# Performance work log

Measured on AMD Instinct MI355X. Metric: run time of the kernel, lower is better.

The kernel has to match this reference:

```python
import jax, jax.numpy as jnp
import numpy as np

DIM = 1024
H = 8            # heads (light and heavy)
DH = 64          # dim_head
W = 64           # local attention window (light_window_size // 2)
NQ = 512         # num_heavy_tokens_q
NKV = 1024       # num_heavy_tokens_kv
EPS = 1.0        # coor descent eps
NITERS = 50      # coor descent iters
FETCH = 9.0 / 8.0
SCALE = DH ** -0.5


def _ln(x, w, b):
    m = x.mean(-1, keepdims=True)
    v = ((x - m) ** 2).mean(-1, keepdims=True)
    return (x - m) * jax.lax.rsqrt(v + 1e-5) * w + b


def _rms(x, g):
    n = jnp.maximum(jnp.linalg.norm(x, axis=-1, keepdims=True), 1e-12)
    return x / n * np.sqrt(DIM).astype(np.float32) * g


def local_attn(x, Wqkv, Wout):
    # LocalMHA, non-causal, look_backward=1, look_forward=1, window W
    b, n, _ = x.shape
    nw = n // W
    qkv = x @ Wqkv.T                      # [b,n,3*H*DH]
    q, k, v = jnp.split(qkv, 3, axis=-1)
    def towin(t):
        return t.reshape(b, nw, W, H, DH).transpose(0, 3, 1, 2, 4)  # [b,h,nw,w,dh]
    q, k, v = map(towin, (q, k, v))
    def expand(t):  # gather prev/cur/next windows -> [b,h,nw,3w,dh]
        tp = jnp.pad(t, ((0, 0), (0, 0), (1, 1), (0, 0), (0, 0)))
        return jnp.concatenate([tp[:, :, :-2], tp[:, :, 1:-1], tp[:, :, 2:]], axis=3)
    ke, ve = expand(k), expand(v)
    sim = jnp.einsum('bhnid,bhnjd->bhnij', q, ke) * SCALE
    win = jnp.arange(nw)
    valid = jnp.concatenate([
        jnp.repeat((win > 0)[:, None], W, 1),
        jnp.ones((nw, W), bool),
        jnp.repeat((win < nw - 1)[:, None], W, 1)], axis=1)  # [nw,3w]
    sim = jnp.where(valid[None, None, :, None, :], sim, -1e9)
    attn = jax.nn.softmax(sim, axis=-1)
    o = jnp.einsum('bhnij,bhnjd->bhnid', attn, ve)
    o = o.transpose(0, 2, 3, 1, 4).reshape(b, n, H * DH)
    return o @ Wout.T


def route(x, routing_token, num_tokens):
    # CoordinateDescentRouter with num_routing_tokens=1, straight_through=True
    s = jnp.einsum('bnd,rd->brn', x, routing_token).reshape(x.shape[0], x.shape[1])
    n = s.shape[-1]
    logk = jnp.log(jnp.asarray(min(num_tokens * FETCH, float(n)), s.dtype))
    def body(ab, _):
        a, bb = ab
        a = EPS * (logk - jax.nn.logsumexp((s + bb) / EPS, axis=-1, keepdims=True))
        bb = -jax.nn.relu(s + a)
        return (a, bb), None
    (a, bb), _ = jax.lax.scan(body, (jnp.zeros((s.shape[0], 1), s.dtype), -s), None, length=NITERS)
    scores = jnp.exp((s + a + bb) / EPS)
    sel_scores, sel_idx = jax.lax.top_k(scores, num_tokens)
    # straight-through: forward value 1.0, gradient of identity
    sel_scores = sel_scores + jax.lax.stop_gradient(1.0 - sel_scores)
    return sel_scores, sel_idx


def heavy_attn(xq, ctx, scores_kv, gamma, Wq, Wkv, Wout, null_kv):
    b = xq.shape[0]
    xq = _rms(xq, gamma)
    ctx = _rms(ctx, gamma)
    q = (xq @ Wq.T).reshape(b, -1, H, DH).transpose(0, 2, 1, 3)           # [b,h,nq,dh]
    kv = (ctx @ Wkv.T).reshape(b, -1, H, 2 * DH).transpose(0, 2, 1, 3)    # [b,h,nkv,2dh]
    k, v = kv[..., :DH], kv[..., DH:]
    v = v * scores_kv[:, None, :, None]
    nk = jnp.broadcast_to(null_kv[0][None, :, None, :], (b, H, 1, DH))
    nv = jnp.broadcast_to(null_kv[1][None, :, None, :], (b, H, 1, DH))
    k = jnp.concatenate([nk, k], axis=2)
    v = jnp.concatenate([nv, v], axis=2)
    sim = jnp.einsum('bhid,bhjd->bhij', q, k) * SCALE
    attn = jax.nn.softmax(sim, axis=-1)
    o = jnp.einsum('bhij,bhjd->bhid', attn, v)
    o = o.transpose(0, 2, 1, 3).reshape(b, -1, H * DH)
    return o @ Wout.T


def setup_inputs() -> dict:
    key = jax.random.key(0)
    ks = jax.random.split(key, 12)
    D, IN = DIM, H * DH
    w = lambda k, shape: jax.random.normal(k, shape, jnp.float32) * 0.02
    return {
        'x': jax.random.normal(ks[0], (4, 4096, D), jnp.float32),
        'ln_w': jnp.ones((D,), jnp.float32),
        'ln_b': jnp.zeros((D,), jnp.float32),
        'Wqkv': w(ks[1], (3 * IN, D)),
        'Wout_l': w(ks[2], (D, IN)),
        'rt_q': jax.random.normal(ks[3], (1, D), jnp.float32),
        'rt_kv': jax.random.normal(ks[4], (1, D), jnp.float32),
        'gamma': jnp.ones((D,), jnp.float32),
        'Wq': w(ks[5], (IN, D)),
        'Wkv': w(ks[6], (2 * IN, D)),
        'Wout_h': w(ks[7], (D, IN)),
        'null_kv': jax.random.normal(ks[8], (2, H, DH), jnp.float32),
        'null_q': jax.random.normal(ks[9], (D,), jnp.float32),
    }


def reference(x, ln_w, ln_b, Wqkv, Wout_l, rt_q, rt_kv, gamma, Wq, Wkv, Wout_h, null_kv, null_q):
    b, n, d = x.shape
    light = local_attn(_ln(x, ln_w, ln_b), Wqkv, Wout_l)
    sq, iq = route(x, rt_q, NQ)
    skv, ikv = route(x, rt_kv, NKV)
    br = jnp.arange(b)[:, None]
    xq = x[br, iq]          # gather routed queries  [b,NQ,d]
    xkv = x[br, ikv]        # gather routed kv       [b,NKV,d]
    heavy = heavy_attn(xq, xkv, skv, gamma, Wq, Wkv, Wout_h, null_kv)
    heavy = heavy * sq[..., None]
    out = jnp.broadcast_to(null_q[None, None, :], (b, n, d))
    out = out.at[br, iq].set(heavy)   # scatter heavy branch back
    return out + light
```

## Files before the change

kernel.cpp:

```cpp
#include <hip/hip_runtime.h>
#include <hip/hip_bf16.h>

typedef __attribute__((ext_vector_type(8))) short bv8;
typedef __attribute__((ext_vector_type(4))) float fv4;
typedef __hip_bfloat16 bf16;

#define MFMA16(a,b,c) __builtin_amdgcn_mfma_f32_16x16x32_bf16((a),(b),(c),0,0,0)
#define GLOAD_LDS(gp, lp) __builtin_amdgcn_global_load_lds( \
    (const __attribute__((address_space(1))) void*)(gp), \
    (__attribute__((address_space(3))) void*)(lp), 16, 0, 0)

template<int NW>
__device__ __forceinline__ float blockReduceSumF(float v) {
  #pragma unroll
  for (int m = 1; m < 64; m <<= 1) v += __shfl_xor(v, m, 64);
  __shared__ float sm[NW];
  if ((threadIdx.x & 63) == 0) sm[threadIdx.x >> 6] = v;
  __syncthreads();
  float t = 0.f;
  #pragma unroll
  for (int i = 0; i < NW; ++i) t += sm[i];
  __syncthreads();
  return t;
}

template<int NW>
__device__ __forceinline__ double blockReduceMaxD(double v) {
  #pragma unroll
  for (int m = 1; m < 64; m <<= 1) v = fmax(v, __shfl_xor(v, m, 64));
  __shared__ double sm[NW];
  if ((threadIdx.x & 63) == 0) sm[threadIdx.x >> 6] = v;
  __syncthreads();
  double t = sm[0];
  #pragma unroll
  for (int i = 1; i < NW; ++i) t = fmax(t, sm[i]);
  __syncthreads();
  return t;
}

__global__ __launch_bounds__(256)
void prep_kernel(const float* __restrict__ x, const float* __restrict__ lnw,
                 const float* __restrict__ lnb, const float* __restrict__ rtq,
                 const float* __restrict__ rtkv, bf16* __restrict__ lnout,
                 double* __restrict__ s,
                 const float* __restrict__ a0, const float* __restrict__ a1,
                 const float* __restrict__ a2, const float* __restrict__ a3,
                 const float* __restrict__ a4,
                 bf16* __restrict__ b0, bf16* __restrict__ b1, bf16* __restrict__ b2,
                 bf16* __restrict__ b3, bf16* __restrict__ b4,
                 int* __restrict__ posq) {
  const int bid = blockIdx.x;
  if (bid < 16384) {
    const int r = bid;
    const float* xr = x + (size_t)r * 1024;
    float v4[4]; float ssum = 0.f;
    double dq = 0.0, dk = 0.0;
    #pragma unroll
    for (int i = 0; i < 4; ++i) {
      int d = threadIdx.x + i * 256;
      float v = xr[d];
      v4[i] = v; ssum += v;
      dq += (double)v * (double)rtq[d];
      dk += (double)v * (double)rtkv[d];
    }
    ssum = blockReduceSumF<4>(ssum);
    const float mean = ssum * (1.0f / 1024.0f);
    float vs = 0.f;
    #pragma unroll
    for (int i = 0; i < 4; ++i) { float d = v4[i] - mean; vs += d * d; }
    vs = blockReduceSumF<4>(vs);
    const float rstd = 1.0f / sqrtf(vs * (1.0f / 1024.0f) + 1e-5f);
    #pragma unroll
    for (int m = 1; m < 64; m <<= 1) { dq += __shfl_xor(dq, m, 64); dk += __shfl_xor(dk, m, 64); }
    __shared__ double smq[4], smk[4];
    if ((threadIdx.x & 63) == 0) { smq[threadIdx.x >> 6] = dq; smk[threadIdx.x >> 6] = dk; }
    __syncthreads();
    if (threadIdx.x == 0) {
      s[r] = smq[0] + smq[1] + smq[2] + smq[3];
      s[16384 + r] = smk[0] + smk[1] + smk[2] + smk[3];
    }
    bf16* orow = lnout + (size_t)r * 1024;
    #pragma unroll
    for (int i = 0; i < 4; ++i) {
      int d = threadIdx.x + i * 256;
      orow[d] = __float2bfloat16((v4[i] - mean) * rstd * lnw[d] + lnb[d]);
    }
  } else if (bid < 18432) {
    size_t g = ((size_t)(bid - 16384) * 256 + threadIdx.x) * 8;
    const float* src; bf16* dst; size_t off;
    if (g < 1572864)      { src = a0; dst = b0; off = g; }
    else if (g < 2097152) { src = a1; dst = b1; off = g - 1572864; }
    else if (g < 2621440) { src = a2; dst = b2; off = g - 2097152; }
    else if (g < 3670016) { src = a3; dst = b3; off = g - 2621440; }
    else                  { src = a4; dst = b4; off = g - 3670016; }
    float4 v0 = *(const float4*)(src + off);
    float4 v1 = *(const float4*)(src + off + 4);
    bv8 o;
    ((bf16*)&o)[0] = __float2bfloat16(v0.x); ((bf16*)&o)[1] = __float2bfloat16(v0.y);
    ((bf16*)&o)[2] = __float2bfloat16(v0.z); ((bf16*)&o)[3] = __float2bfloat16(v0.w);
    ((bf16*)&o)[4] = __float2bfloat16(v1.x); ((bf16*)&o)[5] = __float2bfloat16(v1.y);
    ((bf16*)&o)[6] = __float2bfloat16(v1.z); ((bf16*)&o)[7] = __float2bfloat16(v1.w);
    *(bv8*)(dst + off) = o;
  } else {
    int i0 = (bid - 18432) * 1024 + threadIdx.x * 4;
    posq[i0] = -1; posq[i0 + 1] = -1; posq[i0 + 2] = -1; posq[i0 + 3] = -1;
  }
}

template<int EPI>
__device__ __forceinline__ void gemm_core(
    const bf16* __restrict__ A, const bf16* __restrict__ B, void* __restrict__ Cout,
    int N, int K, int row0, int col0, bf16* As, bf16* Bs,
    const int* __restrict__ posq, const float* __restrict__ nullq) {
  const int tid = threadIdx.x;
  const int lane = tid & 63, w = tid >> 6;
  const int wr = w >> 1, wc = w & 1;
  const int lrow = lane & 15, lk = (lane >> 4) * 8;
  fv4 acc[4][4];
  #pragma unroll
  for (int m = 0; m < 4; ++m)
    #pragma unroll
    for (int n = 0; n < 4; ++n) acc[m][n] = (fv4){0.f, 0.f, 0.f, 0.f};
  const int ob0 = w * 2048;
  for (int k0 = 0; k0 < K; k0 += 32) {
    #pragma unroll
    for (int t = 0; t < 2; ++t) {
      int ob = ob0 + t * 1024;
      int ofl = ob + lane * 16;
      int r = ofl >> 6, c8 = ((ofl >> 4) & 3) * 8;
      GLOAD_LDS(A + (size_t)(row0 + r) * K + k0 + c8, (char*)As + ob);
      GLOAD_LDS(B + (size_t)(col0 + r) * K + k0 + c8, (char*)Bs + ob);
    }
    __syncthreads();
    bv8 af[4], bfr[4];
    #pragma unroll
    for (int m = 0; m < 4; ++m) af[m] = *(bv8*)&As[(wr * 64 + m * 16 + lrow) * 32 + lk];
    #pragma unroll
    for (int n = 0; n < 4; ++n) bfr[n] = *(bv8*)&Bs[(wc * 64 + n * 16 + lrow) * 32 + lk];
    #pragma unroll
    for (int m = 0; m < 4; ++m)
      #pragma unroll
      for (int n = 0; n < 4; ++n)
        acc[m][n] = MFMA16(af[m], bfr[n], acc[m][n]);
    __syncthreads();
  }
  #pragma unroll
  for (int m = 0; m < 4; ++m) {
    int gr0 = row0 + wr * 64 + m * 16 + (lane >> 4) * 4;
    #pragma unroll
    for (int n = 0; n < 4; ++n) {
      int gc = col0 + wc * 64 + n * 16 + lrow;
      #pragma unroll
      for (int r = 0; r < 4; ++r) {
        int grow = gr0 + r;
        float vv = acc[m][n][r];
        if (EPI == 0) {
          ((bf16*)Cout)[(size_t)grow * N + gc] = __float2bfloat16(vv);
        } else {
          float add = (posq[grow] >= 0) ? 0.0f : nullq[gc];
          ((float*)Cout)[(size_t)grow * N + gc] = vv + add;
        }
      }
    }
  }
}

__device__ __forceinline__ void xcd_remap(int d, int gx, int& row0, int& col0) {
  int q = d >> 3;
  col0 = (q % gx) * 128;
  row0 = ((d & 7) + 8 * (q / gx)) * 128;
}

__global__ __launch_bounds__(256)
void qkv_route_kernel(const bf16* __restrict__ ln, const bf16* __restrict__ Wqkv,
                      bf16* __restrict__ qkv,
                      const double* __restrict__ s_all, int* __restrict__ iq,
                      int* __restrict__ ikv, int* __restrict__ posq,
                      unsigned long long* __restrict__ keys_ws) {
  __shared__ alignas(16) bf16 As[128 * 32];
  __shared__ alignas(16) bf16 Bs[128 * 32];
  __shared__ int scn[256];
  __shared__ double red[4];
  const int bid = blockIdx.x;
  const int tid = threadIdx.x;
  if (bid >= 8) {
    int row0, col0;
    xcd_remap(bid - 8, 12, row0, col0);
    gemm_core<0>(ln, Wqkv, qkv, 1536, 1024, row0, col0, As, Bs, nullptr, nullptr);
  } else {
    const int route = bid >> 2, b = bid & 3;
    const double* s = s_all + route * 16384 + b * 4096;
    const double Kk = (route == 0) ? 576.0 : 1152.0;
    const int KSEL = (route == 0) ? 512 : 1024;
    const int lane = tid & 63, wid = tid >> 6;
    double sv[16];
    #pragma unroll
    for (int i = 0; i < 16; ++i) sv[i] = s[tid * 16 + i];
    double mx = sv[0];
    #pragma unroll
    for (int i = 1; i < 16; ++i) mx = fmax(mx, sv[i]);
    mx = blockReduceMaxD<4>(mx);
    double ev[16];
    #pragma unroll
    for (int i = 0; i < 16; ++i) ev[i] = exp(sv[i] - mx);
    double z = (4096.0 / Kk) * exp(-mx);
    for (int it = 1; it < 50; ++it) {
      double t0 = 0.0, t1 = 0.0;
      #pragma unroll
      for (int i = 0; i < 16; i += 2) { t0 += fmin(ev[i], z); t1 += fmin(ev[i + 1], z); }
      double t = t0 + t1;
      #pragma unroll
      for (int m = 1; m < 64; m <<= 1) t += __shfl_xor(t, m, 64);
      if (lane == 0) red[wid] = t;
      __syncthreads();
      z = (red[0] + red[1] + red[2] + red[3]) / Kk;
      __syncthreads();
    }
    const double a = -mx - log(z);
    float scf[16]; int m16 = 0;
    #pragma unroll
    for (int i = 0; i < 16; ++i) {
      scf[i] = (float)exp(fmin(sv[i] + a, 0.0));
      m16 += (scf[i] == 1.0f) ? 1 : 0;
    }
    scn[tid] = m16;
    __syncthreads();
    for (int off = 1; off < 256; off <<= 1) {
      int v = (tid >= off) ? scn[tid - off] : 0;
      __syncthreads();
      scn[tid] += v;
      __syncthreads();
    }
    const int total = scn[255];
    const int excl = scn[tid] - m16;
    if (total >= KSEL) {
      int rk = excl;
      #pragma unroll
      for (int i = 0; i < 16; ++i) {
        if (scf[i] == 1.0f) {
          if (rk < KSEL) {
            int idx = tid * 16 + i;
            if (route == 0) { iq[b * 512 + rk] = idx; posq[b * 4096 + idx] = rk; }
            else            { ikv[b * 1024 + rk] = idx; }
          }
          rk++;
        }
      }
    } else {
      unsigned long long* keys = keys_ws + (size_t)bid * 4096;
      #pragma unroll
      for (int i = 0; i < 16; ++i) {
        unsigned bits = __float_as_uint(scf[i]);
        keys[tid * 16 + i] = ((unsigned long long)(~bits) << 32) | (unsigned long long)(tid * 16 + i);
      }
      for (int k = 2; k <= 4096; k <<= 1) {
        for (int j = k >> 1; j > 0; j >>= 1) {
          __syncthreads();
          for (int t = tid; t < 2048; t += 256) {
            int i2 = ((t & ~(j - 1)) << 1) | (t & (j - 1));
            int ip = i2 + j;
            unsigned long long av = keys[i2], bvv = keys[ip];
            bool up = ((i2 & k) == 0);
            if (up ? (av > bvv) : (av < bvv)) { keys[i2] = bvv; keys[ip] = av; }
          }
        }
      }
      __syncthreads();
      for (int j2 = tid; j2 < KSEL; j2 += 256) {
        int idx = (int)(keys[j2] & 0xFFFFFFFFull);
        if (route == 0) { iq[b * 512 + j2] = idx; posq[b * 4096 + idx] = j2; }
        else            { ikv[b * 1024 + j2] = idx; }
      }
    }
  }
}

__global__ __launch_bounds__(256)
void la_gather_kernel(const bf16* __restrict__ qkv, bf16* __restrict__ olight,
                      const float* __restrict__ x, const float* __restrict__ gamma,
                      const int* __restrict__ iq, const int* __restrict__ ikv,
                      bf16* __restrict__ xq, bf16* __restrict__ xkv) {
  __shared__ bf16 Qs[64][72], Ks[64][72], Vts[64][72], Ps[64][72];
  const int tid = threadIdx.x;
  if (blockIdx.x < 2048) {
    const int w = blockIdx.x & 63, h = (blockIdx.x >> 6) & 7, b = blockIdx.x >> 9;
    const int lane = tid & 63, wv = tid >> 6;
    const int lrow = lane & 15, lkg = lane >> 4;
    {
      const size_t baseq = ((size_t)(b * 4096 + w * 64)) * 1536 + h * 64;
      #pragma unroll
      for (int v = 0; v < 2; ++v) {
        int vec = tid + v * 256; int i = vec >> 3, dd = (vec & 7) * 8;
        *(bv8*)&Qs[i][dd] = *(const bv8*)&qkv[baseq + (size_t)i * 1536 + dd];
      }
    }
    fv4 oacc[4];
    float m_run[4], l_run[4];
    #pragma unroll
    for (int n = 0; n < 4; ++n) oacc[n] = (fv4){0.f, 0.f, 0.f, 0.f};
    #pragma unroll
    for (int r = 0; r < 4; ++r) { m_run[r] = -INFINITY; l_run[r] = 0.f; }
    for (int c = 0; c < 3; ++c) {
      int sw = w - 1 + c;
      if (sw < 0 || sw >= 64) continue;
      __syncthreads();
      const size_t bkv = ((size_t)(b * 4096 + sw * 64)) * 1536 + h * 64;
      #pragma unroll
      for (int v = 0; v < 2; ++v) {
        int vec = tid + v * 256; int i = vec >> 3, dd = (vec & 7) * 8;
        *(bv8*)&Ks[i][dd] = *(const bv8*)&qkv[bkv + 512 + (size_t)i * 1536 + dd];
      }
      #pragma unroll
      for (int v = 0; v < 2; ++v) {
        int vec = tid + v * 256; int j = vec >> 3, d0 = (vec & 7) * 8;
        bv8 val = *(const bv8*)&qkv[bkv + 1024 + (size_t)j * 1536 + d0];
        #pragma unroll
        for (int i = 0; i < 8; ++i) Vts[d0 + i][j] = ((bf16*)&val)[i];
      }
      __syncthreads();
      fv4 sa[4];
      #pragma unroll
      for (int n = 0; n < 4; ++n) {
        sa[n] = (fv4){0.f, 0.f, 0.f, 0.f};
        #pragma unroll
        for (int ks = 0; ks < 2; ++ks) {
          bv8 aq = *(bv8*)&Qs[wv * 16 + lrow][lkg * 8 + ks * 32];
          bv8 bk = *(bv8*)&Ks[n * 16 + lrow][lkg * 8 + ks * 32];
          sa[n] = MFMA16(aq, bk, sa[n]);
        }
      }
      float mc[4];
      #pragma unroll
      for (int r = 0; r < 4; ++r) {
        #pragma unroll
        for (int n = 0; n < 4; ++n) sa[n][r] *= 0.125f;
        mc[r] = fmaxf(fmaxf(sa[0][r], sa[1][r]), fmaxf(sa[2][r], sa[3][r]));
      }
      #pragma unroll
      for (int m = 1; m < 16; m <<= 1)
        #pragma unroll
        for (int r = 0; r < 4; ++r) mc[r] = fmaxf(mc[r], __shfl_xor(mc[r], m, 64));
      float p[4][4], ls[4];
      #pragma unroll
      for (int r = 0; r < 4; ++r) {
        float mn = fmaxf(m_run[r], mc[r]);
        float scl = expf(m_run[r] - mn);
        ls[r] = 0.f;
        #pragma unroll
        for (int n = 0; n < 4; ++n) { p[n][r] = expf(sa[n][r] - mn); ls[r] += p[n][r]; }
        m_run[r] = mn;
        l_run[r] *= scl;
        #pragma unroll
        for (int n = 0; n < 4; ++n) oacc[n][r] *= scl;
      }
      #pragma unroll
      for (int m = 1; m < 16; m <<= 1)
        #pragma unroll
        for (int r = 0; r < 4; ++r) ls[r] += __shfl_xor(ls[r], m, 64);
      #pragma unroll
      for (int r = 0; r < 4; ++r) l_run[r] += ls[r];
      #pragma unroll
      for (int n = 0; n < 4; ++n)
        #pragma unroll
        for (int r = 0; r < 4; ++r)
          Ps[wv * 16 + lkg * 4 + r][n * 16 + lrow] = __float2bfloat16(p[n][r]);
      __syncthreads();
      #pragma unroll
      for (int n = 0; n < 4; ++n)
        #pragma unroll
        for (int ks = 0; ks < 2; ++ks) {
          bv8 ap = *(bv8*)&Ps[wv * 16 + lrow][lkg * 8 + ks * 32];
          bv8 bvv = *(bv8*)&Vts[n * 16 + lrow][lkg * 8 + ks * 32];
          oacc[n] = MFMA16(ap, bvv, oacc[n]);
        }
    }
    const size_t ob = ((size_t)(b * 4096 + w * 64 + wv * 16)) * 512 + h * 64;
    #pragma unroll
    for (int n = 0; n < 4; ++n)
      #pragma unroll
      for (int r = 0; r < 4; ++r) {
        int row = lkg * 4 + r;
        olight[ob + (size_t)row * 512 + n * 16 + lrow] = __float2bfloat16(oacc[n][r] / l_run[r]);
      }
  } else {
    const int gid = blockIdx.x - 2048;
    const float* src; bf16* dst;
    if (gid < 2048) {
      int b = gid >> 9, j = gid & 511;
      int tok = iq[b * 512 + j];
      src = x + ((size_t)(b * 4096 + tok)) * 1024;
      dst = xq + (size_t)gid * 1024;
    } else {
      int id = gid - 2048;
      int b = id >> 10, j = id & 1023;
      int tok = ikv[b * 1024 + j];
      src = x + ((size_t)(b * 4096 + tok)) * 1024;
      dst = xkv + (size_t)id * 1024;
    }
    float v4[4]; float ss = 0.f;
    #pragma unroll
    for (int i = 0; i < 4; ++i) { v4[i] = src[tid + i * 256]; ss += v4[i] * v4[i]; }
    ss = blockReduceSumF<4>(ss);
    const float nrm = fmaxf(sqrtf(ss), 1e-12f);
    const float scl = 32.0f / nrm;
    #pragma unroll
    for (int i = 0; i < 4; ++i) {
      int d = tid + i * 256;
      dst[d] = __float2bfloat16(v4[i] * scl * gamma[d]);
    }
  }
}

__global__ __launch_bounds__(256)
void lightout_wqkv_kernel(const bf16* __restrict__ ol, const bf16* __restrict__ Woutl,
                          float* __restrict__ out,
                          const int* __restrict__ posq, const float* __restrict__ nq,
                          const bf16* __restrict__ xkv, const bf16* __restrict__ Wkv,
                          bf16* __restrict__ kvh,
                          const bf16* __restrict__ xq, const bf16* __restrict__ Wq,
                          bf16* __restrict__ qh) {
  __shared__ alignas(16) bf16 As[128 * 32];
  __shared__ alignas(16) bf16 Bs[128 * 32];
  const int bid = blockIdx.x;
  int row0, col0;
  if (bid < 256) {
    xcd_remap(bid, 8, row0, col0);
    gemm_core<0>(xkv, Wkv, kvh, 1024, 1024, row0, col0, As, Bs, nullptr, nullptr);
  } else if (bid < 320) {
    xcd_remap(bid - 256, 4, row0, col0);
    gemm_core<0>(xq, Wq, qh, 512, 1024, row0, col0, As, Bs, nullptr, nullptr);
  } else {
    xcd_remap(bid - 320, 8, row0, col0);
    gemm_core<2>(ol, Woutl, out, 1024, 512, row0, col0, As, Bs, posq, nq);
  }
}

__global__ __launch_bounds__(256)
void heavy_attn_split_kernel(const bf16* __restrict__ qh, const bf16* __restrict__ kvh,
                             const float* __restrict__ nkv, bf16* __restrict__ o_part,
                             float* __restrict__ ml_part) {
  const int qt = blockIdx.x, h = blockIdx.y;
  const int b = blockIdx.z >> 2, s = blockIdx.z & 3;
  const int tid = threadIdx.x;
  const int lane = tid & 63, wv = tid >> 6;
  const int lrow = lane & 15, lkg = lane >> 4;
  __shared__ bf16 Qs[64][72], Ks[64][72], Vts[64][72], Ps[64][72];
  {
    const size_t baseq = ((size_t)(b * 512 + qt * 64)) * 512 + h * 64;
    #pragma unroll
    for (int v = 0; v < 2; ++v) {
      int vec = tid + v * 256; int i = vec >> 3, dd = (vec & 7) * 8;
      *(bv8*)&Qs[i][dd] = *(const bv8*)&qh[baseq + (size_t)i * 512 + dd];
    }
  }
  fv4 oacc[4];
  float m_run[4], l_run[4];
  #pragma unroll
  for (int n = 0; n < 4; ++n) oacc[n] = (fv4){0.f, 0.f, 0.f, 0.f};
  #pragma unroll
  for (int r = 0; r < 4; ++r) { m_run[r] = -INFINITY; l_run[r] = 0.f; }
  const int cs = (s == 0) ? 0 : (s * 4 + 1);
  const int ce = s * 4 + 5;
  for (int c = cs; c < ce; ++c) {
    __syncthreads();
    #pragma unroll
    for (int v = 0; v < 2; ++v) {
      int vec = tid + v * 256; int j = vec >> 3, dd = (vec & 7) * 8;
      int kvg = c * 64 + j;
      bv8 val;
      if (kvg >= 1 && kvg <= 1024) {
        val = *(const bv8*)&kvh[((size_t)(b * 1024 + kvg - 1)) * 1024 + h * 128 + dd];
      } else if (kvg == 0) {
        #pragma unroll
        for (int t = 0; t < 8; ++t) ((bf16*)&val)[t] = __float2bfloat16(nkv[h * 64 + dd + t]);
      } else {
        #pragma unroll
        for (int t = 0; t < 8; ++t) ((short*)&val)[t] = 0;
      }
      *(bv8*)&Ks[j][dd] = val;
    }
    #pragma unroll
    for (int v = 0; v < 2; ++v) {
      int vec = tid + v * 256; int j = vec >> 3, d0 = (vec & 7) * 8;
      int kvg = c * 64 + j;
      if (kvg >= 1 && kvg <= 1024) {
        bv8 val = *(const bv8*)&kvh[((size_t)(b * 1024 + kvg - 1)) * 1024 + h * 128 + 64 + d0];
        #pragma unroll
        for (int i = 0; i < 8; ++i) Vts[d0 + i][j] = ((bf16*)&val)[i];
      } else if (kvg == 0) {
        #pragma unroll
        for (int i = 0; i < 8; ++i) Vts[d0 + i][j] = __float2bfloat16(nkv[512 + h * 64 + d0 + i]);
      } else {
        #pragma unroll
        for (int i = 0; i < 8; ++i) Vts[d0 + i][j] = __float2bfloat16(0.0f);
      }
    }
    __syncthreads();
    fv4 sa[4];
    #pragma unroll
    for (int n = 0; n < 4; ++n) {
      sa[n] = (fv4){0.f, 0.f, 0.f, 0.f};
      #pragma unroll
      for (int ks = 0; ks < 2; ++ks) {
        bv8 aq = *(bv8*)&Qs[wv * 16 + lrow][lkg * 8 + ks * 32];
        bv8 bk = *(bv8*)&Ks[n * 16 + lrow][lkg * 8 + ks * 32];
        sa[n] = MFMA16(aq, bk, sa[n]);
      }
    }
    float mc[4];
    #pragma unroll
    for (int r = 0; r < 4; ++r) {
      #pragma unroll
      for (int n = 0; n < 4; ++n) {
        sa[n][r] *= 0.125f;
        int kvg = c * 64 + n * 16 + lrow;
        if (kvg > 1024) sa[n][r] = -1e30f;
      }
      mc[r] = fmaxf(fmaxf(sa[0][r], sa[1][r]), fmaxf(sa[2][r], sa[3][r]));
    }
    #pragma unroll
    for (int m = 1; m < 16; m <<= 1)
      #pragma unroll
      for (int r = 0; r < 4; ++r) mc[r] = fmaxf(mc[r], __shfl_xor(mc[r], m, 64));
    float p[4][4], ls[4];
    #pragma unroll
    for (int r = 0; r < 4; ++r) {
      float mn = fmaxf(m_run[r], mc[r]);
      float scl = expf(m_run[r] - mn);
      ls[r] = 0.f;
      #pragma unroll
      for (int n = 0; n < 4; ++n) { p[n][r] = expf(sa[n][r] - mn); ls[r] += p[n][r]; }
      m_run[r] = mn;
      l_run[r] *= scl;
      #pragma unroll
      for (int n = 0; n < 4; ++n) oacc[n][r] *= scl;
    }
    #pragma unroll
    for (int m = 1; m < 16; m <<= 1)
      #pragma unroll
      for (int r = 0; r < 4; ++r) ls[r] += __shfl_xor(ls[r], m, 64);
    #pragma unroll
    for (int r = 0; r < 4; ++r) l_run[r] += ls[r];
    #pragma unroll
    for (int n = 0; n < 4; ++n)
      #pragma unroll
      for (int r = 0; r < 4; ++r)
        Ps[wv * 16 + lkg * 4 + r][n * 16 + lrow] = __float2bfloat16(p[n][r]);
    __syncthreads();
    #pragma unroll
    for (int n = 0; n < 4; ++n)
      #pragma unroll
      for (int ks = 0; ks < 2; ++ks) {
        bv8 ap = *(bv8*)&Ps[wv * 16 + lrow][lkg * 8 + ks * 32];
        bv8 bvv = *(bv8*)&Vts[n * 16 + lrow][lkg * 8 + ks * 32];
        oacc[n] = MFMA16(ap, bvv, oacc[n]);
      }
  }
  const int idx = (((s * 4 + b) * 8 + h) * 8 + qt);
  bf16* ob = o_part + (size_t)idx * 4096;
  #pragma unroll
  for (int n = 0; n < 4; ++n)
    #pragma unroll
    for (int r = 0; r < 4; ++r) {
      int row = wv * 16 + lkg * 4 + r;
      ob[row * 64 + n * 16 + lrow] = __float2bfloat16(oacc[n][r]);
    }
  if (lrow == 0) {
    #pragma unroll
    for (int r = 0; r < 4; ++r) {
      int row = wv * 16 + lkg * 4 + r;
      ml_part[idx * 128 + row] = m_run[r];
      ml_part[idx * 128 + 64 + row] = l_run[r];
    }
  }
}

__global__ __launch_bounds__(256)
void wouth_scatter_kernel(const bf16* __restrict__ o_part, const float* __restrict__ ml_part,
                          const bf16* __restrict__ B, float* __restrict__ out,
                          const int* __restrict__ iq) {
  __shared__ alignas(16) bf16 As[128 * 32];
  __shared__ alignas(16) bf16 Bs[128 * 32];
  const int N = 1024, K = 512;
  int row0, col0;
  xcd_remap(blockIdx.y * gridDim.x + blockIdx.x, gridDim.x, row0, col0);
  const int tid = threadIdx.x;
  const int lane = tid & 63, w = tid >> 6;
  const int wr = w >> 1, wc = w & 1;
  const int lrow = lane & 15, lk = (lane >> 4) * 8;
  fv4 acc[4][4];
  #pragma unroll
  for (int m = 0; m < 4; ++m)
    #pragma unroll
    for (int n = 0; n < 4; ++n) acc[m][n] = (fv4){0.f, 0.f, 0.f, 0.f};
  const int ob0 = w * 2048;
  for (int k0 = 0; k0 < K; k0 += 32) {
    #pragma unroll
    for (int t = 0; t < 2; ++t) {
      int ob = ob0 + t * 1024;
      int ofl = ob + lane * 16;
      int r = ofl >> 6, c8 = ((ofl >> 4) & 3) * 8;
      int grow = row0 + r, k = k0 + c8;
      int b = grow >> 9, qrow = grow & 511;
      int qt = qrow >> 6, row_in = qrow & 63;
      int h = k >> 6, d0 = k & 63;
      bv8 v[4]; float m[4], l[4];
      #pragma unroll
      for (int s = 0; s < 4; ++s) {
        int idx = (((s * 4 + b) * 8 + h) * 8 + qt);
        v[s] = *(const bv8*)&o_part[(size_t)idx * 4096 + row_in * 64 + d0];
        m[s] = ml_part[idx * 128 + row_in];
        l[s] = ml_part[idx * 128 + 64 + row_in];
      }
      float mstar = fmaxf(fmaxf(m[0], m[1]), fmaxf(m[2], m[3]));
      float ws[4]; float wsum = 0.f;
      #pragma unroll
      for (int s = 0; s < 4; ++s) { ws[s] = expf(m[s] - mstar); wsum += ws[s] * l[s]; }
      const float inv = 1.0f / wsum;
      bv8 o8;
      #pragma unroll
      for (int j = 0; j < 8; ++j) {
        float acc8 = 0.f;
        #pragma unroll
        for (int s = 0; s < 4; ++s) acc8 += ws[s] * __bfloat162float(((bf16*)&v[s])[j]);
        ((bf16*)&o8)[j] = __float2bfloat16(acc8 * inv);
      }
      *(bv8*)((char*)As + ofl) = o8;
      GLOAD_LDS(B + (size_t)(col0 + r) * K + k0 + c8, (char*)Bs + ob);
    }
    __syncthreads();
    bv8 af[4], bfr[4];
    #pragma unroll
    for (int m2 = 0; m2 < 4; ++m2) af[m2] = *(bv8*)&As[(wr * 64 + m2 * 16 + lrow) * 32 + lk];
    #pragma unroll
    for (int n = 0; n < 4; ++n) bfr[n] = *(bv8*)&Bs[(wc * 64 + n * 16 + lrow) * 32 + lk];
    #pragma unroll
    for (int m2 = 0; m2 < 4; ++m2)
      #pragma unroll
      for (int n = 0; n < 4; ++n)
        acc[m2][n] = MFMA16(af[m2], bfr[n], acc[m2][n]);
    __syncthreads();
  }
  #pragma unroll
  for (int m2 = 0; m2 < 4; ++m2) {
    int gr0 = row0 + wr * 64 + m2 * 16 + (lane >> 4) * 4;
    #pragma unroll
    for (int n = 0; n < 4; ++n) {
      int gc = col0 + wc * 64 + n * 16 + lrow;
      #pragma unroll
      for (int r = 0; r < 4; ++r) {
        int grow = gr0 + r;
        int b = grow >> 9;
        int tok = iq[grow];
        float* op = out + ((size_t)(b * 4096 + tok)) * 1024 + gc;
        *op += acc[m2][n][r];
      }
    }
  }
}

extern "C" void kernel_launch(void* const* d_in, const int* in_sizes, int n_in,
                              void* d_out, int out_size, void* d_ws, size_t ws_size,
                              hipStream_t stream) {
  (void)in_sizes; (void)n_in; (void)out_size; (void)ws_size;
  const float* x     = (const float*)d_in[0];
  const float* ln_w  = (const float*)d_in[1];
  const float* ln_b  = (const float*)d_in[2];
  const float* Wqkv  = (const float*)d_in[3];
  const float* Woutl = (const float*)d_in[4];
  const float* rtq   = (const float*)d_in[5];
  const float* rtkv  = (const float*)d_in[6];
  const float* gamma = (const float*)d_in[7];
  const float* Wq    = (const float*)d_in[8];
  const float* Wkv   = (const float*)d_in[9];
  const float* Wouth = (const float*)d_in[10];
  const float* nkv   = (const float*)d_in[11];
  const float* nq    = (const float*)d_in[12];
  float* out = (float*)d_out;

  char* ws = (char*)d_ws;
  size_t off = 0;
  auto alloc = [&](size_t bytes) -> void* {
    void* p = ws + off;
    off = (off + bytes + 255) & ~(size_t)255;
    return p;
  };
  bf16* ln_bf    = (bf16*)alloc(16384ull * 1024 * 2);
  bf16* qkv_bf   = (bf16*)alloc(16384ull * 1536 * 2);
  bf16* ol_bf    = (bf16*)alloc(16384ull * 512 * 2);
  bf16* Wqkv_bf  = (bf16*)alloc(1536ull * 1024 * 2);
  bf16* Woutl_bf = (bf16*)alloc(1024ull * 512 * 2);
  bf16* Wq_bf    = (bf16*)alloc(512ull * 1024 * 2);
  bf16* Wkv_bf   = (bf16*)alloc(1024ull * 1024 * 2);
  bf16* Wouth_bf = (bf16*)alloc(1024ull * 512 * 2);
  double* s_d    = (double*)alloc(32768ull * 8);
  int* iq        = (int*)alloc(2048ull * 4);
  int* ikv       = (int*)alloc(4096ull * 4);
  int* posq      = (int*)alloc(16384ull * 4);
  bf16* xq_bf    = (bf16*)alloc(2048ull * 1024 * 2);
  bf16* xkv_bf   = (bf16*)alloc(4096ull * 1024 * 2);
  bf16* qh_bf    = (bf16*)alloc(2048ull * 512 * 2);
  bf16* kvh_bf   = (bf16*)alloc(4096ull * 1024 * 2);
  bf16* o_part   = (bf16*)alloc(4096ull * 4096 * 2);
  float* ml_part = (float*)alloc(4096ull * 128 * 4);
  unsigned long long* keys_ws = (unsigned long long*)alloc(8ull * 4096 * 8);

  prep_kernel<<<18448, 256, 0, stream>>>(x, ln_w, ln_b, rtq, rtkv, ln_bf, s_d,
                                         Wqkv, Woutl, Wq, Wkv, Wouth,
                                         Wqkv_bf, Woutl_bf, Wq_bf, Wkv_bf, Wouth_bf,
                                         posq);

  qkv_route_kernel<<<1544, 256, 0, stream>>>(ln_bf, Wqkv_bf, qkv_bf,
                                             s_d, iq, ikv, posq, keys_ws);

  la_gather_kernel<<<8192, 256, 0, stream>>>(qkv_bf, ol_bf, x, gamma, iq, ikv, xq_bf, xkv_bf);

  lightout_wqkv_kernel<<<1344, 256, 0, stream>>>(ol_bf, Woutl_bf, out, posq, nq,
                                                 xkv_bf, Wkv_bf, kvh_bf,
                                                 xq_bf, Wq_bf, qh_bf);

  heavy_attn_split_kernel<<<dim3(8, 8, 16), 256, 0, stream>>>(qh_bf, kvh_bf, nkv, o_part, ml_part);

  wouth_scatter_kernel<<<dim3(8, 16), 256, 0, stream>>>(o_part, ml_part, Wouth_bf, out, iq);
}
```

Before: 299.7 us.

## Move light-output GEMM from the projection kernel into the heavy attention launch

The light-branch output projection GEMM (1024 blocks) moves out of the combined Wq/Wkv projection kernel and into the heavy attention kernel launch. The heavy attention blocks and the light GEMM blocks now share one grid, with shared memory carved from a common arena. The Wq/Wkv projection becomes a small 320-block launch. The aim is to fill idle CUs during heavy attention with independent GEMM work and so shorten the critical path. In exchange, the small projection kernel may underfill the GPU, and the merged kernel's register and LDS use is set by whichever branch needs more.

```diff
diff --git a/kernel.cpp b/kernel.cpp
--- a/kernel.cpp
+++ b/kernel.cpp
@@ -412,13 +412,10 @@
 }
 
 __global__ __launch_bounds__(256)
-void lightout_wqkv_kernel(const bf16* __restrict__ ol, const bf16* __restrict__ Woutl,
-                          float* __restrict__ out,
-                          const int* __restrict__ posq, const float* __restrict__ nq,
-                          const bf16* __restrict__ xkv, const bf16* __restrict__ Wkv,
-                          bf16* __restrict__ kvh,
-                          const bf16* __restrict__ xq, const bf16* __restrict__ Wq,
-                          bf16* __restrict__ qh) {
+void wqkv_kernel(const bf16* __restrict__ xkv, const bf16* __restrict__ Wkv,
+                 bf16* __restrict__ kvh,
+                 const bf16* __restrict__ xq, const bf16* __restrict__ Wq,
+                 bf16* __restrict__ qh) {
   __shared__ alignas(16) bf16 As[128 * 32];
   __shared__ alignas(16) bf16 Bs[128 * 32];
   const int bid = blockIdx.x;
@@ -426,152 +423,166 @@
   if (bid < 256) {
     xcd_remap(bid, 8, row0, col0);
     gemm_core<0>(xkv, Wkv, kvh, 1024, 1024, row0, col0, As, Bs, nullptr, nullptr);
-  } else if (bid < 320) {
+  } else {
     xcd_remap(bid - 256, 4, row0, col0);
     gemm_core<0>(xq, Wq, qh, 512, 1024, row0, col0, As, Bs, nullptr, nullptr);
+  }
+}
+
+__global__ __launch_bounds__(256)
+void heavy_lightout_kernel(const bf16* __restrict__ qh, const bf16* __restrict__ kvh,
+                           const float* __restrict__ nkv, bf16* __restrict__ o_part,
+                           float* __restrict__ ml_part,
+                           const bf16* __restrict__ ol, const bf16* __restrict__ Woutl,
+                           float* __restrict__ out,
+                           const int* __restrict__ posq, const float* __restrict__ nq) {
+  __shared__ __align__(16) char arena[36864];
+  const int tid = threadIdx.x;
+  const int bid = blockIdx.x;
+  if (bid < 1024) {
+    const int qt = bid & 7, h = (bid >> 3) & 7, z = bid >> 6;
+    const int b = z >> 2, s = z & 3;
+    const int lane = tid & 63, wv = tid >> 6;
+    const int lrow = lane & 15, lkg = lane >> 4;
+    typedef bf16 row72[72];
+    row72* Qs  = (row72*)arena;
+    row72* Ks  = (row72*)(arena + 9216);
+    row72* Vts = (row72*)(arena + 18432);
+    row72* Ps  = (row72*)(arena + 27648);
+    {
+      const size_t baseq = ((size_t)(b * 512 + qt * 64)) * 512 + h * 64;
+      #pragma unroll
+      for (int v = 0; v < 2; ++v) {
+        int vec = tid + v * 256; int i = vec >> 3, dd = (vec & 7) * 8;
+        *(bv8*)&Qs[i][dd] = *(const bv8*)&qh[baseq + (size_t)i * 512 + dd];
+      }
+    }
+    fv4 oacc[4];
+    float m_run[4], l_run[4];
+    #pragma unroll
+    for (int n = 0; n < 4; ++n) oacc[n] = (fv4){0.f, 0.f, 0.f, 0.f};
+    #pragma unroll
+    for (int r = 0; r < 4; ++r) { m_run[r] = -INFINITY; l_run[r] = 0.f; }
+    const int cs = (s == 0) ? 0 : (s * 4 + 1);
+    const int ce = s * 4 + 5;
+    for (int c = cs; c < ce; ++c) {
+      __syncthreads();
+      #pragma unroll
+      for (int v = 0; v < 2; ++v) {
+        int vec = tid + v * 256; int j = vec >> 3, dd = (vec & 7) * 8;
+        int kvg = c * 64 + j;
+        bv8 val;
+        if (kvg >= 1 && kvg <= 1024) {
+          val = *(const bv8*)&kvh[((size_t)(b * 1024 + kvg - 1)) * 1024 + h * 128 + dd];
+        } else if (kvg == 0) {
+          #pragma unroll
+          for (int t = 0; t < 8; ++t) ((bf16*)&val)[t] = __float2bfloat16(nkv[h * 64 + dd + t]);
+        } else {
+          #pragma unroll
+          for (int t = 0; t < 8; ++t) ((short*)&val)[t] = 0;
+        }
+        *(bv8*)&Ks[j][dd] = val;
+      }
+      #pragma unroll
+      for (int v = 0; v < 2; ++v) {
+        int vec = tid + v * 256; int j = vec >> 3, d0 = (vec & 7) * 8;
+        int kvg = c * 64 + j;
+        if (kvg >= 1 && kvg <= 1024) {
+          bv8 val = *(const bv8*)&kvh[((size_t)(b * 1024 + kvg - 1)) * 1024 + h * 128 + 64 + d0];
+          #pragma unroll
+          for (int i = 0; i < 8; ++i) Vts[d0 + i][j] = ((bf16*)&val)[i];
+        } else if (kvg == 0) {
+          #pragma unroll
+          for (int i = 0; i < 8; ++i) Vts[d0 + i][j] = __float2bfloat16(nkv[512 + h * 64 + d0 + i]);
+        } else {
+          #pragma unroll
+          for (int i = 0; i < 8; ++i) Vts[d0 + i][j] = __float2bfloat16(0.0f);
+        }
+      }
+      __syncthreads();
+      fv4 sa[4];
+      #pragma unroll
+      for (int n = 0; n < 4; ++n) {
+        sa[n] = (fv4){0.f, 0.f, 0.f, 0.f};
+        #pragma unroll
+        for (int ks = 0; ks < 2; ++ks) {
+          bv8 aq = *(bv8*)&Qs[wv * 16 + lrow][lkg * 8 + ks * 32];
+          bv8 bk = *(bv8*)&Ks[n * 16 + lrow][lkg * 8 + ks * 32];
+          sa[n] = MFMA16(aq, bk, sa[n]);
+        }
+      }
+      float mc[4];
+      #pragma unroll
+      for (int r = 0; r < 4; ++r) {
+        #pragma unroll
+        for (int n = 0; n < 4; ++n) {
+          sa[n][r] *= 0.125f;
+          int kvg = c * 64 + n * 16 + lrow;
+          if (kvg > 1024) sa[n][r] = -1e30f;
+        }
+        mc[r] = fmaxf(fmaxf(sa[0][r], sa[1][r]), fmaxf(sa[2][r], sa[3][r]));
+      }
+      #pragma unroll
+      for (int m = 1; m < 16; m <<= 1)
+        #pragma unroll
+        for (int r = 0; r < 4; ++r) mc[r] = fmaxf(mc[r], __shfl_xor(mc[r], m, 64));
+      float p[4][4], ls[4];
+      #pragma unroll
+      for (int r = 0; r < 4; ++r) {
+        float mn = fmaxf(m_run[r], mc[r]);
+        float scl = expf(m_run[r] - mn);
+        ls[r] = 0.f;
+        #pragma unroll
+        for (int n = 0; n < 4; ++n) { p[n][r] = expf(sa[n][r] - mn); ls[r] += p[n][r]; }
+        m_run[r] = mn;
+        l_run[r] *= scl;
+        #pragma unroll
+        for (int n = 0; n < 4; ++n) oacc[n][r] *= scl;
+      }
+      #pragma unroll
+      for (int m = 1; m < 16; m <<= 1)
+        #pragma unroll
+        for (int r = 0; r < 4; ++r) ls[r] += __shfl_xor(ls[r], m, 64);
+      #pragma unroll
+      for (int r = 0; r < 4; ++r) l_run[r] += ls[r];
+      #pragma unroll
+      for (int n = 0; n < 4; ++n)
+        #pragma unroll
+        for (int r = 0; r < 4; ++r)
+          Ps[wv * 16 + lkg * 4 + r][n * 16 + lrow] = __float2bfloat16(p[n][r]);
+      __syncthreads();
+      #pragma unroll
+      for (int n = 0; n < 4; ++n)
+        #pragma unroll
+        for (int ks = 0; ks < 2; ++ks) {
+          bv8 ap = *(bv8*)&Ps[wv * 16 + lrow][lkg * 8 + ks * 32];
+          bv8 bvv = *(bv8*)&Vts[n * 16 + lrow][lkg * 8 + ks * 32];
+          oacc[n] = MFMA16(ap, bvv, oacc[n]);
+        }
+    }
+    const int idx = (((s * 4 + b) * 8 + h) * 8 + qt);
+    bf16* ob = o_part + (size_t)idx * 4096;
+    #pragma unroll
+    for (int n = 0; n < 4; ++n)
+      #pragma unroll
+      for (int r = 0; r < 4; ++r) {
+        int row = wv * 16 + lkg * 4 + r;
+        ob[row * 64 + n * 16 + lrow] = __float2bfloat16(oacc[n][r]);
+      }
+    if (lrow == 0) {
+      #pragma unroll
+      for (int r = 0; r < 4; ++r) {
+        int row = wv * 16 + lkg * 4 + r;
+        ml_part[idx * 128 + row] = m_run[r];
+        ml_part[idx * 128 + 64 + row] = l_run[r];
+      }
+    }
   } else {
-    xcd_remap(bid - 320, 8, row0, col0);
+    bf16* As = (bf16*)arena;
+    bf16* Bs = (bf16*)(arena + 8192);
+    int row0, col0;
+    xcd_remap(bid - 1024, 8, row0, col0);
     gemm_core<2>(ol, Woutl, out, 1024, 512, row0, col0, As, Bs, posq, nq);
-  }
-}
-
-__global__ __launch_bounds__(256)
-void heavy_attn_split_kernel(const bf16* __restrict__ qh, const bf16* __restrict__ kvh,
-                             const float* __restrict__ nkv, bf16* __restrict__ o_part,
-                             float* __restrict__ ml_part) {
-  const int qt = blockIdx.x, h = blockIdx.y;
-  const int b = blockIdx.z >> 2, s = blockIdx.z & 3;
-  const int tid = threadIdx.x;
-  const int lane = tid & 63, wv = tid >> 6;
-  const int lrow = lane & 15, lkg = lane >> 4;
-  __shared__ bf16 Qs[64][72], Ks[64][72], Vts[64][72], Ps[64][72];
-  {
-    const size_t baseq = ((size_t)(b * 512 + qt * 64)) * 512 + h * 64;
-    #pragma unroll
-    for (int v = 0; v < 2; ++v) {
-      int vec = tid + v * 256; int i = vec >> 3, dd = (vec & 7) * 8;
-      *(bv8*)&Qs[i][dd] = *(const bv8*)&qh[baseq + (size_t)i * 512 + dd];
-    }
-  }
-  fv4 oacc[4];
-  float m_run[4], l_run[4];
-  #pragma unroll
-  for (int n = 0; n < 4; ++n) oacc[n] = (fv4){0.f, 0.f, 0.f, 0.f};
-  #pragma unroll
-  for (int r = 0; r < 4; ++r) { m_run[r] = -INFINITY; l_run[r] = 0.f; }
-  const int cs = (s == 0) ? 0 : (s * 4 + 1);
-  const int ce = s * 4 + 5;
-  for (int c = cs; c < ce; ++c) {
-    __syncthreads();
-    #pragma unroll
-    for (int v = 0; v < 2; ++v) {
-      int vec = tid + v * 256; int j = vec >> 3, dd = (vec & 7) * 8;
-      int kvg = c * 64 + j;
-      bv8 val;
-      if (kvg >= 1 && kvg <= 1024) {
-        val = *(const bv8*)&kvh[((size_t)(b * 1024 + kvg - 1)) * 1024 + h * 128 + dd];
-      } else if (kvg == 0) {
-        #pragma unroll
-        for (int t = 0; t < 8; ++t) ((bf16*)&val)[t] = __float2bfloat16(nkv[h * 64 + dd + t]);
-      } else {
-        #pragma unroll
-        for (int t = 0; t < 8; ++t) ((short*)&val)[t] = 0;
-      }
-      *(bv8*)&Ks[j][dd] = val;
-    }
-    #pragma unroll
-    for (int v = 0; v < 2; ++v) {
-      int vec = tid + v * 256; int j = vec >> 3, d0 = (vec & 7) * 8;
-      int kvg = c * 64 + j;
-      if (kvg >= 1 && kvg <= 1024) {
-        bv8 val = *(const bv8*)&kvh[((size_t)(b * 1024 + kvg - 1)) * 1024 + h * 128 + 64 + d0];
-        #pragma unroll
-        for (int i = 0; i < 8; ++i) Vts[d0 + i][j] = ((bf16*)&val)[i];
-      } else if (kvg == 0) {
-        #pragma unroll
-        for (int i = 0; i < 8; ++i) Vts[d0 + i][j] = __float2bfloat16(nkv[512 + h * 64 + d0 + i]);
-      } else {
-        #pragma unroll
-        for (int i = 0; i < 8; ++i) Vts[d0 + i][j] = __float2bfloat16(0.0f);
-      }
-    }
-    __syncthreads();
-    fv4 sa[4];
-    #pragma unroll
-    for (int n = 0; n < 4; ++n) {
-      sa[n] = (fv4){0.f, 0.f, 0.f, 0.f};
-      #pragma unroll
-      for (int ks = 0; ks < 2; ++ks) {
-        bv8 aq = *(bv8*)&Qs[wv * 16 + lrow][lkg * 8 + ks * 32];
-        bv8 bk = *(bv8*)&Ks[n * 16 + lrow][lkg * 8 + ks * 32];
-        sa[n] = MFMA16(aq, bk, sa[n]);
-      }
-    }
-    float mc[4];
-    #pragma unroll
-    for (int r = 0; r < 4; ++r) {
-      #pragma unroll
-      for (int n = 0; n < 4; ++n) {
-        sa[n][r] *= 0.125f;
-        int kvg = c * 64 + n * 16 + lrow;
-        if (kvg > 1024) sa[n][r] = -1e30f;
-      }
-      mc[r] = fmaxf(fmaxf(sa[0][r], sa[1][r]), fmaxf(sa[2][r], sa[3][r]));
-    }
-    #pragma unroll
-    for (int m = 1; m < 16; m <<= 1)
-      #pragma unroll
-      for (int r = 0; r < 4; ++r) mc[r] = fmaxf(mc[r], __shfl_xor(mc[r], m, 64));
-    float p[4][4], ls[4];
-    #pragma unroll
-    for (int r = 0; r < 4; ++r) {
-      float mn = fmaxf(m_run[r], mc[r]);
-      float scl = expf(m_run[r] - mn);
-      ls[r] = 0.f;
-      #pragma unroll
-      for (int n = 0; n < 4; ++n) { p[n][r] = expf(sa[n][r] - mn); ls[r] += p[n][r]; }
-      m_run[r] = mn;
-      l_run[r] *= scl;
-      #pragma unroll
-      for (int n = 0; n < 4; ++n) oacc[n][r] *= scl;
-    }
-    #pragma unroll
-    for (int m = 1; m < 16; m <<= 1)
-      #pragma unroll
-      for (int r = 0; r < 4; ++r) ls[r] += __shfl_xor(ls[r], m, 64);
-    #pragma unroll
-    for (int r = 0; r < 4; ++r) l_run[r] += ls[r];
-    #pragma unroll
-    for (int n = 0; n < 4; ++n)
-      #pragma unroll
-      for (int r = 0; r < 4; ++r)
-        Ps[wv * 16 + lkg * 4 + r][n * 16 + lrow] = __float2bfloat16(p[n][r]);
-    __syncthreads();
-    #pragma unroll
-    for (int n = 0; n < 4; ++n)
-      #pragma unroll
-      for (int ks = 0; ks < 2; ++ks) {
-        bv8 ap = *(bv8*)&Ps[wv * 16 + lrow][lkg * 8 + ks * 32];
-        bv8 bvv = *(bv8*)&Vts[n * 16 + lrow][lkg * 8 + ks * 32];
-        oacc[n] = MFMA16(ap, bvv, oacc[n]);
-      }
-  }
-  const int idx = (((s * 4 + b) * 8 + h) * 8 + qt);
-  bf16* ob = o_part + (size_t)idx * 4096;
-  #pragma unroll
-  for (int n = 0; n < 4; ++n)
-    #pragma unroll
-    for (int r = 0; r < 4; ++r) {
-      int row = wv * 16 + lkg * 4 + r;
-      ob[row * 64 + n * 16 + lrow] = __float2bfloat16(oacc[n][r]);
-    }
-  if (lrow == 0) {
-    #pragma unroll
-    for (int r = 0; r < 4; ++r) {
-      int row = wv * 16 + lkg * 4 + r;
-      ml_part[idx * 128 + row] = m_run[r];
-      ml_part[idx * 128 + 64 + row] = l_run[r];
-    }
   }
 }
 
@@ -715,11 +726,10 @@
 
   la_gather_kernel<<<8192, 256, 0, stream>>>(qkv_bf, ol_bf, x, gamma, iq, ikv, xq_bf, xkv_bf);
 
-  lightout_wqkv_kernel<<<1344, 256, 0, stream>>>(ol_bf, Woutl_bf, out, posq, nq,
-                                                 xkv_bf, Wkv_bf, kvh_bf,
-                                                 xq_bf, Wq_bf, qh_bf);
-
-  heavy_attn_split_kernel<<<dim3(8, 8, 16), 256, 0, stream>>>(qh_bf, kvh_bf, nkv, o_part, ml_part);
+  wqkv_kernel<<<320, 256, 0, stream>>>(xkv_bf, Wkv_bf, kvh_bf, xq_bf, Wq_bf, qh_bf);
+
+  heavy_lightout_kernel<<<2048, 256, 0, stream>>>(qh_bf, kvh_bf, nkv, o_part, ml_part,
+                                                  ol_bf, Woutl_bf, out, posq, nq);
 
   wouth_scatter_kernel<<<dim3(8, 16), 256, 0, stream>>>(o_part, ml_part, Wouth_bf, out, iq);
 }
```

Result: no change. 298.9 us (-0.3%).
